# Kernel optimization log

Hardware: AMD Instinct MI355X
Metric: run time of the kernel (lower is better)

## Reference

```python
import jax, jax.numpy as jnp
import numpy as np

BS, SEQ, NV, DM, K = 128, 2048, 64, 512, 64
MAX_ITER, TOL = 10, 1e-4


def setup_inputs() -> dict:
    key = jax.random.key(0)
    k1, k2, k3, k4 = jax.random.split(key, 4)
    x = jax.random.normal(k1, (BS, SEQ, NV), jnp.float32)
    bound = 1.0 / np.sqrt(SEQ)
    W = jax.random.uniform(k2, (DM, SEQ), jnp.float32, -bound, bound)  # nn.Linear weight
    b = jax.random.uniform(k3, (DM,), jnp.float32, -bound, bound)
    centroids = jax.random.normal(k4, (K, DM), jnp.float32)  # kaiming-uniform-init param (random stand-in)
    return {"x": x, "W": W, "b": b, "centroids": centroids}


def _kmeans(x_emb, centroids):
    # x_emb: [N, DM]; fixed-length scan with a `done` flag emulating torch's tol break.
    N = x_emb.shape[0]
    x_sq = jnp.sum(x_emb * x_emb, axis=1, keepdims=True)  # [N,1]

    def body(state, _):
        cent, ids, done = state
        # squared euclidean distances (argmin-equivalent to cdist p=2)
        d2 = x_sq - 2.0 * (x_emb @ cent.T) + jnp.sum(cent * cent, axis=1)  # [N,K]
        new_ids = jnp.argmin(d2, axis=1)
        sums = jax.ops.segment_sum(x_emb, new_ids, num_segments=K)          # [K,DM]
        counts = jax.ops.segment_sum(jnp.ones((N,), x_emb.dtype), new_ids, num_segments=K)
        means = sums / jnp.maximum(counts, 1.0)[:, None]
        new_cent = jnp.where((counts > 0)[:, None], means, cent)  # empty cluster keeps old centroid
        shift = jnp.linalg.norm(new_cent - cent)
        cent_out = jnp.where(done, cent, new_cent)
        ids_out = jnp.where(done, ids, new_ids)
        done_out = done | (shift < TOL)
        return (cent_out, ids_out, done_out), None

    init = (centroids, jnp.zeros((N,), jnp.int32), jnp.array(False))
    (cent, ids, _), _ = jax.lax.scan(body, init, None, length=MAX_ITER)
    return ids, cent


def reference(x, W, b, centroids):
    # x: [bs, seq, n_vars] -> permute -> linear(seq->d_model) -> [bs*n_vars, d_model]
    xt = jnp.transpose(x, (0, 2, 1))                 # [bs, n_vars, seq]
    x_emb = (xt @ W.T + b).reshape(-1, DM)           # [bs*n_vars, d_model]
    ids, cent = _kmeans(x_emb, centroids)
    prob = jax.nn.one_hot(ids, K, dtype=jnp.float32).reshape(BS, NV, K)
    return prob, cent, x_emb
```

## Files before the change

### kernel.cpp

```cpp
#include <hip/hip_runtime.h>

#define SEQ 2048
#define NVAR 64
#define DMODEL 512
#define BSZ 128
#define KC 64
#define NPT (BSZ*NVAR)
#define MAXIT 10

typedef __bf16 bf16x8 __attribute__((ext_vector_type(8)));
typedef float f32x4 __attribute__((ext_vector_type(4)));

__device__ __forceinline__ void load_lds16(const void* g, void* l) {
  __builtin_amdgcn_global_load_lds((const __attribute__((address_space(1))) void*)g,
                                   (__attribute__((address_space(3))) void*)l, 16, 0, 0);
}

__device__ __forceinline__ unsigned short bf16_rn(float x) {
  unsigned int u = __float_as_uint(x);
  u += 0x7fffu + ((u >> 16) & 1u);
  return (unsigned short)(u >> 16);
}

__global__ __launch_bounds__(256) void init_k(const float* __restrict__ c0,
    float* __restrict__ cent, unsigned short* __restrict__ centh,
    unsigned short* __restrict__ centl, float* __restrict__ csq4,
    int* __restrict__ done, float* __restrict__ shift2, int* __restrict__ ticket) {
  const int k = blockIdx.x, t = threadIdx.x;
  __shared__ float red[256];
  float v0, v1;
  {
    int d = t;
    v0 = c0[k * DMODEL + d];
    cent[k * DMODEL + d] = v0;
    unsigned short h = bf16_rn(v0);
    centh[k * DMODEL + d] = h;
    centl[k * DMODEL + d] = bf16_rn(v0 - __uint_as_float((unsigned)h << 16));
  }
  {
    int d = t + 256;
    v1 = c0[k * DMODEL + d];
    cent[k * DMODEL + d] = v1;
    unsigned short h = bf16_rn(v1);
    centh[k * DMODEL + d] = h;
    centl[k * DMODEL + d] = bf16_rn(v1 - __uint_as_float((unsigned)h << 16));
  }
  red[t] = v0 * v0; __syncthreads();
  for (int s = 64; s > 0; s >>= 1) { if ((t & 127) < s) red[t] += red[t + s]; __syncthreads(); }
  if (t == 0)   csq4[0 * KC + k] = red[0];
  if (t == 128) csq4[1 * KC + k] = red[128];
  __syncthreads();
  red[t] = v1 * v1; __syncthreads();
  for (int s = 64; s > 0; s >>= 1) { if ((t & 127) < s) red[t] += red[t + s]; __syncthreads(); }
  if (t == 0)   csq4[2 * KC + k] = red[0];
  if (t == 128) csq4[3 * KC + k] = red[128];
  if (k == 0 && t < MAXIT) { shift2[t] = 0.f; ticket[t] = 0; }
  if (k == 0 && t == 31) *done = 0;
}

__global__ __launch_bounds__(256) void conv_w(const float* __restrict__ W,
    unsigned short* __restrict__ Wh, unsigned short* __restrict__ Wl) {
  int i = (blockIdx.x * 256 + threadIdx.x) * 4;
  float4 v = *(const float4*)(W + i);
  ushort4 h, l;
  h.x = bf16_rn(v.x); l.x = bf16_rn(v.x - __uint_as_float((unsigned)h.x << 16));
  h.y = bf16_rn(v.y); l.y = bf16_rn(v.y - __uint_as_float((unsigned)h.y << 16));
  h.z = bf16_rn(v.z); l.z = bf16_rn(v.z - __uint_as_float((unsigned)h.z << 16));
  h.w = bf16_rn(v.w); l.w = bf16_rn(v.w - __uint_as_float((unsigned)h.w << 16));
  *(ushort4*)(Wh + i) = h;
  *(ushort4*)(Wl + i) = l;
}

__global__ __launch_bounds__(256) void conv_x(const float* __restrict__ x,
    unsigned short* __restrict__ Xh, unsigned short* __restrict__ Xl) {
  __shared__ float tile[64 * 65];
  const int k0 = blockIdx.x * 64;
  const int bs = blockIdx.y;
  const int t = threadIdx.x;
  const float* xb = x + (size_t)bs * SEQ * NVAR + (size_t)k0 * NVAR;
  #pragma unroll
  for (int p = 0; p < 4; ++p) {
    int idx = t + 256 * p;
    int row = idx >> 4, c4 = (idx & 15) * 4;
    float4 v = *(const float4*)(xb + row * NVAR + c4);
    tile[row * 65 + c4 + 0] = v.x; tile[row * 65 + c4 + 1] = v.y;
    tile[row * 65 + c4 + 2] = v.z; tile[row * 65 + c4 + 3] = v.w;
  }
  __syncthreads();
  const int v = t >> 2;
  const int kc = (t & 3) * 16;
  unsigned short h[16], l[16];
  #pragma unroll
  for (int j = 0; j < 16; ++j) {
    float f = tile[(kc + j) * 65 + v];
    h[j] = bf16_rn(f);
    l[j] = bf16_rn(f - __uint_as_float((unsigned)h[j] << 16));
  }
  size_t off = (size_t)(bs * 64 + v) * SEQ + k0 + kc;
  *(uint4*)(Xh + off)     = *(uint4*)&h[0];
  *(uint4*)(Xh + off + 8) = *(uint4*)&h[8];
  *(uint4*)(Xl + off)     = *(uint4*)&l[0];
  *(uint4*)(Xl + off + 8) = *(uint4*)&l[8];
}

__global__ __launch_bounds__(256) void gemm_mfma(
    const unsigned short* __restrict__ Ah, const unsigned short* __restrict__ Al,
    const unsigned short* __restrict__ Bh, const unsigned short* __restrict__ Bl,
    const float* __restrict__ bias, float* __restrict__ emb) {
  __shared__ unsigned short sAh[32 * 64] __attribute__((aligned(16)));
  __shared__ unsigned short sAl[32 * 64] __attribute__((aligned(16)));
  __shared__ unsigned short sBh[256 * 64] __attribute__((aligned(16)));
  __shared__ unsigned short sBl[256 * 64] __attribute__((aligned(16)));
  const int t = threadIdx.x;
  const int w = t >> 6, lane = t & 63;
  const int m0 = blockIdx.x * 32;
  const int n0 = blockIdx.y * 256;
  const int wn = w * 64;
  const int lrow = lane >> 3, sl8 = lane & 7;
  const int csrc = sl8 ^ lrow;

  f32x4 acc[2][4];
  #pragma unroll
  for (int i = 0; i < 2; ++i)
    #pragma unroll
    for (int j = 0; j < 4; ++j) acc[i][j] = (f32x4){0.f, 0.f, 0.f, 0.f};

  for (int kt = 0; kt < SEQ; kt += 64) {
    __syncthreads();
    {
      const int r = w * 8 + lrow;
      const size_t ga = (size_t)(m0 + r) * SEQ + kt + csrc * 8;
      load_lds16(Ah + ga, &sAh[r * 64 + sl8 * 8]);
      load_lds16(Al + ga, &sAl[r * 64 + sl8 * 8]);
    }
    #pragma unroll
    for (int i = 0; i < 8; ++i) {
      const int r = w * 64 + i * 8 + lrow;
      const size_t gb = (size_t)(n0 + r) * SEQ + kt + csrc * 8;
      load_lds16(Bh + gb, &sBh[r * 64 + sl8 * 8]);
      load_lds16(Bl + gb, &sBl[r * 64 + sl8 * 8]);
    }
    __syncthreads();
    #pragma unroll
    for (int kk = 0; kk < 2; ++kk) {
      const int sl = ((kk * 4 + (lane >> 4)) ^ (lane & 7)) * 8;
      bf16x8 ah[2], al[2], bh[4], bl[4];
      #pragma unroll
      for (int mi = 0; mi < 2; ++mi) {
        int off = (mi * 16 + (lane & 15)) * 64 + sl;
        ah[mi] = *(const bf16x8*)&sAh[off];
        al[mi] = *(const bf16x8*)&sAl[off];
      }
      #pragma unroll
      for (int ni = 0; ni < 4; ++ni) {
        int off = (wn + ni * 16 + (lane & 15)) * 64 + sl;
        bh[ni] = *(const bf16x8*)&sBh[off];
        bl[ni] = *(const bf16x8*)&sBl[off];
      }
      #pragma unroll
      for (int mi = 0; mi < 2; ++mi)
        #pragma unroll
        for (int ni = 0; ni < 4; ++ni) {
          acc[mi][ni] = __builtin_amdgcn_mfma_f32_16x16x32_bf16(ah[mi], bh[ni], acc[mi][ni], 0, 0, 0);
          acc[mi][ni] = __builtin_amdgcn_mfma_f32_16x16x32_bf16(ah[mi], bl[ni], acc[mi][ni], 0, 0, 0);
          acc[mi][ni] = __builtin_amdgcn_mfma_f32_16x16x32_bf16(al[mi], bh[ni], acc[mi][ni], 0, 0, 0);
        }
    }
  }
  #pragma unroll
  for (int ni = 0; ni < 4; ++ni) {
    const int n = n0 + wn + ni * 16 + (lane & 15);
    const float bv = bias[n];
    #pragma unroll
    for (int mi = 0; mi < 2; ++mi) {
      const int m = m0 + mi * 16 + (lane >> 4) * 4;
      #pragma unroll
      for (int r = 0; r < 4; ++r)
        emb[(size_t)(m + r) * DMODEL + n] = acc[mi][ni][r] + bv;
    }
  }
}

__global__ __launch_bounds__(256) void gemm_emb(const float* __restrict__ x,
    const float* __restrict__ W, const float* __restrict__ bias,
    float* __restrict__ emb) {
  __shared__ float As[64][64];
  __shared__ float Ws[64][132];
  const int bs = blockIdx.y;
  const int n0 = blockIdx.x * 128;
  const int t = threadIdx.x;
  const int tx = t & 15, ty = t >> 4;
  float bv[8];
  #pragma unroll
  for (int j = 0; j < 8; ++j) bv[j] = bias[n0 + 8 * tx + j];
  float acc[4][8];
  #pragma unroll
  for (int i = 0; i < 4; ++i)
    #pragma unroll
    for (int j = 0; j < 8; ++j) acc[i][j] = 0.f;
  const float* xb = x + (size_t)bs * SEQ * NVAR;
  for (int k0 = 0; k0 < SEQ; k0 += 64) {
    __syncthreads();
    {
      const float4* src = (const float4*)(xb + (size_t)k0 * NVAR);
      float4* dst = (float4*)&As[0][0];
      #pragma unroll
      for (int r = 0; r < 4; ++r) dst[t + 256 * r] = src[t + 256 * r];
    }
    #pragma unroll
    for (int r = 0; r < 8; ++r) {
      int idx = t + 256 * r;
      int k4 = idx & 15, n = idx >> 4;
      float4 wv = *(const float4*)(W + (size_t)(n0 + n) * SEQ + k0 + 4 * k4);
      Ws[4 * k4 + 0][n] = wv.x; Ws[4 * k4 + 1][n] = wv.y;
      Ws[4 * k4 + 2][n] = wv.z; Ws[4 * k4 + 3][n] = wv.w;
    }
    __syncthreads();
    #pragma unroll 8
    for (int kk = 0; kk < 64; ++kk) {
      const float4 a  = *(const float4*)&As[kk][4 * ty];
      const float4 w0 = *(const float4*)&Ws[kk][8 * tx];
      const float4 w1 = *(const float4*)&Ws[kk][8 * tx + 4];
      const float av[4] = {a.x, a.y, a.z, a.w};
      const float wv[8] = {w0.x, w0.y, w0.z, w0.w, w1.x, w1.y, w1.z, w1.w};
      #pragma unroll
      for (int i = 0; i < 4; ++i)
        #pragma unroll
        for (int j = 0; j < 8; ++j)
          acc[i][j] = fmaf(av[i], wv[j], acc[i][j]);
    }
  }
  #pragma unroll
  for (int i = 0; i < 4; ++i) {
    int row = bs * NVAR + 4 * ty + i;
    float4 o0 = make_float4(acc[i][0] + bv[0], acc[i][1] + bv[1],
                            acc[i][2] + bv[2], acc[i][3] + bv[3]);
    float4 o1 = make_float4(acc[i][4] + bv[4], acc[i][5] + bv[5],
                            acc[i][6] + bv[6], acc[i][7] + bv[7]);
    *(float4*)(emb + (size_t)row * DMODEL + n0 + 8 * tx) = o0;
    *(float4*)(emb + (size_t)row * DMODEL + n0 + 8 * tx + 4) = o1;
  }
}

__global__ __launch_bounds__(256) void conv_et(const float* __restrict__ emb,
    unsigned short* __restrict__ Eh, unsigned short* __restrict__ El,
    unsigned short* __restrict__ Eth, unsigned short* __restrict__ Etl) {
  __shared__ unsigned short Lh[64][72];
  __shared__ unsigned short Ll[64][72];
  const int d0 = blockIdx.x * 64;
  const int p0 = blockIdx.y * 64;
  const int t = threadIdx.x;
  #pragma unroll
  for (int q = 0; q < 2; ++q) {
    int idx = t + 256 * q;
    int r = idx >> 3, c = idx & 7;
    const float* src = emb + (size_t)(p0 + r) * DMODEL + d0 + c * 8;
    float4 v0 = *(const float4*)src;
    float4 v1 = *(const float4*)(src + 4);
    unsigned short h[8], l[8];
    const float vv[8] = {v0.x, v0.y, v0.z, v0.w, v1.x, v1.y, v1.z, v1.w};
    #pragma unroll
    for (int j = 0; j < 8; ++j) {
      h[j] = bf16_rn(vv[j]);
      l[j] = bf16_rn(vv[j] - __uint_as_float((unsigned)h[j] << 16));
    }
    size_t eo = (size_t)(p0 + r) * DMODEL + d0 + c * 8;
    *(uint4*)(Eh + eo) = *(uint4*)&h[0];
    *(uint4*)(El + eo) = *(uint4*)&l[0];
    *(uint4*)&Lh[r][c * 8] = *(uint4*)&h[0];
    *(uint4*)&Ll[r][c * 8] = *(uint4*)&l[0];
  }
  __syncthreads();
  #pragma unroll
  for (int q = 0; q < 2; ++q) {
    int idx = t + 256 * q;
    int dd = idx >> 3, pc = idx & 7;
    unsigned short h[8], l[8];
    #pragma unroll
    for (int j = 0; j < 8; ++j) {
      h[j] = Lh[pc * 8 + j][dd];
      l[j] = Ll[pc * 8 + j][dd];
    }
    size_t to = (size_t)(d0 + dd) * NPT + p0 + pc * 8;
    *(uint4*)(Eth + to) = *(uint4*)&h[0];
    *(uint4*)(Etl + to) = *(uint4*)&l[0];
  }
}

__global__ __launch_bounds__(256) void k12_fused(
    const unsigned short* __restrict__ Eh, const unsigned short* __restrict__ El,
    const unsigned short* __restrict__ Eth, const unsigned short* __restrict__ Etl,
    const unsigned short* __restrict__ Ch, const unsigned short* __restrict__ Cl,
    const float* __restrict__ csq4, const int* __restrict__ done,
    int* __restrict__ ids, float* __restrict__ pcnt, float* __restrict__ psum) {
  if (*done) return;
  __shared__ __align__(16) unsigned char smem[98304];
  __shared__ float csq_l[64];
  __shared__ int cnt_l[64];
  __shared__ int ids_l[128];
  const int t = threadIdx.x;
  const int w = t >> 6, lane = t & 63;
  const int g = blockIdx.x & 63, dq = blockIdx.x >> 6;
  const int p0 = g * 128;
  const int lrow = lane >> 3, sl8 = lane & 7;
  const int csrc = sl8 ^ lrow;

  if (t < 64) {
    csq_l[t] = csq4[t] + csq4[KC + t] + csq4[2 * KC + t] + csq4[3 * KC + t];
    cnt_l[t] = 0;
  }
  __syncthreads();

#define STAGE_A(B, KT) do { \
    unsigned short* bEh = (unsigned short*)(smem + (B) * 49152); \
    unsigned short* bEl = (unsigned short*)(smem + (B) * 49152 + 16384); \
    unsigned short* bCh = (unsigned short*)(smem + (B) * 49152 + 32768); \
    unsigned short* bCl = (unsigned short*)(smem + (B) * 49152 + 40960); \
    _Pragma("unroll") \
    for (int i_ = 0; i_ < 4; ++i_) { \
      const int r_ = w * 32 + i_ * 8 + lrow; \
      const size_t ga_ = (size_t)(p0 + r_) * DMODEL + (KT) + csrc * 8; \
      load_lds16(Eh + ga_, &bEh[r_ * 64 + sl8 * 8]); \
      load_lds16(El + ga_, &bEl[r_ * 64 + sl8 * 8]); \
    } \
    _Pragma("unroll") \
    for (int i_ = 0; i_ < 2; ++i_) { \
      const int r_ = w * 16 + i_ * 8 + lrow; \
      const size_t gc_ = (size_t)r_ * DMODEL + (KT) + csrc * 8; \
      load_lds16(Ch + gc_, &bCh[r_ * 64 + sl8 * 8]); \
      load_lds16(Cl + gc_, &bCl[r_ * 64 + sl8 * 8]); \
    } \
  } while (0)

#define COMPUTE_A(B) do { \
    const unsigned short* bEh = (const unsigned short*)(smem + (B) * 49152); \
    const unsigned short* bEl = (const unsigned short*)(smem + (B) * 49152 + 16384); \
    const unsigned short* bCh = (const unsigned short*)(smem + (B) * 49152 + 32768); \
    const unsigned short* bCl = (const unsigned short*)(smem + (B) * 49152 + 40960); \
    _Pragma("unroll") \
    for (int kk = 0; kk < 2; ++kk) { \
      const int sl = ((kk * 4 + (lane >> 4)) ^ (lane & 7)) * 8; \
      bf16x8 eh[2], el[2], ch[4], cl[4]; \
      _Pragma("unroll") \
      for (int mi = 0; mi < 2; ++mi) { \
        int off = (w * 32 + mi * 16 + (lane & 15)) * 64 + sl; \
        eh[mi] = *(const bf16x8*)&bEh[off]; \
        el[mi] = *(const bf16x8*)&bEl[off]; \
      } \
      _Pragma("unroll") \
      for (int ni = 0; ni < 4; ++ni) { \
        int off = (ni * 16 + (lane & 15)) * 64 + sl; \
        ch[ni] = *(const bf16x8*)&bCh[off]; \
        cl[ni] = *(const bf16x8*)&bCl[off]; \
      } \
      _Pragma("unroll") \
      for (int mi = 0; mi < 2; ++mi) \
        _Pragma("unroll") \
        for (int ni = 0; ni < 4; ++ni) { \
          acc[mi][ni] = __builtin_amdgcn_mfma_f32_16x16x32_bf16(eh[mi], ch[ni], acc[mi][ni], 0, 0, 0); \
          acc[mi][ni] = __builtin_amdgcn_mfma_f32_16x16x32_bf16(eh[mi], cl[ni], acc[mi][ni], 0, 0, 0); \
          acc[mi][ni] = __builtin_amdgcn_mfma_f32_16x16x32_bf16(el[mi], ch[ni], acc[mi][ni], 0, 0, 0); \
        } \
    } \
  } while (0)

  f32x4 acc[2][4];
  #pragma unroll
  for (int i = 0; i < 2; ++i)
    #pragma unroll
    for (int j = 0; j < 4; ++j) acc[i][j] = (f32x4){0.f, 0.f, 0.f, 0.f};

  STAGE_A(0, 0);
  for (int kt8 = 0; kt8 < 8; kt8 += 2) {
    STAGE_A(1, (kt8 + 1) * 64);
    asm volatile("s_waitcnt vmcnt(12)" ::: "memory");
    __builtin_amdgcn_s_barrier();
    __builtin_amdgcn_sched_barrier(0);
    COMPUTE_A(0);
    __builtin_amdgcn_s_barrier();
    if (kt8 + 2 < 8) {
      STAGE_A(0, (kt8 + 2) * 64);
      asm volatile("s_waitcnt vmcnt(12)" ::: "memory");
    } else {
      asm volatile("s_waitcnt vmcnt(0)" ::: "memory");
    }
    __builtin_amdgcn_s_barrier();
    __builtin_amdgcn_sched_barrier(0);
    COMPUTE_A(1);
    __builtin_amdgcn_s_barrier();
  }

  #pragma unroll
  for (int mi = 0; mi < 2; ++mi) {
    #pragma unroll
    for (int r = 0; r < 4; ++r) {
      float bv = csq_l[lane & 15] - 2.f * acc[mi][0][r];
      int bk = lane & 15;
      #pragma unroll
      for (int ni = 1; ni < 4; ++ni) {
        const int k = ni * 16 + (lane & 15);
        float v = csq_l[k] - 2.f * acc[mi][ni][r];
        if (v < bv) { bv = v; bk = k; }
      }
      #pragma unroll
      for (int m = 1; m < 16; m <<= 1) {
        float ov = __shfl_xor(bv, m, 64);
        int   ok = __shfl_xor(bk, m, 64);
        if (ov < bv || (ov == bv && ok < bk)) { bv = ov; bk = ok; }
      }
      if ((lane & 15) == 0) {
        const int p = w * 32 + mi * 16 + (lane >> 4) * 4 + r;
        ids_l[p] = bk;
        atomicAdd(&cnt_l[bk], 1);
      }
    }
  }
  __syncthreads();
  if (dq == 0) {
    if (t < 128) ids[p0 + t] = ids_l[t];
    if (t < 64) pcnt[g * KC + t] = (float)cnt_l[t];
  }

#define STAGE_B(B, KT) do { \
    unsigned short* bTh = (unsigned short*)(smem + 17408 + (B) * 32768); \
    unsigned short* bTl = (unsigned short*)(smem + 17408 + (B) * 32768 + 16384); \
    _Pragma("unroll") \
    for (int i_ = 0; i_ < 4; ++i_) { \
      const int rr_ = w * 32 + i_ * 8 + lrow; \
      const size_t gt_ = (size_t)(dq * 128 + rr_) * NPT + g * 128 + (KT) + csrc * 8; \
      load_lds16(Eth + gt_, &bTh[rr_ * 64 + sl8 * 8]); \
      load_lds16(Etl + gt_, &bTl[rr_ * 64 + sl8 * 8]); \
    } \
  } while (0)

#define COMPUTE_B(B, KT) do { \
    const unsigned short* bTh = (const unsigned short*)(smem + 17408 + (B) * 32768); \
    const unsigned short* bTl = (const unsigned short*)(smem + 17408 + (B) * 32768 + 16384); \
    _Pragma("unroll") \
    for (int kk = 0; kk < 2; ++kk) { \
      const int quad = lane >> 4; \
      const int poff = (KT) + kk * 32 + quad * 8; \
      bf16x8 a[4], bh[2], bl[2]; \
      _Pragma("unroll") \
      for (int mi = 0; mi < 4; ++mi) \
        a[mi] = *(const bf16x8*)&sOH[(mi * 16 + (lane & 15)) * 136 + poff]; \
      const int sl = ((kk * 4 + quad) ^ (lane & 7)) * 8; \
      _Pragma("unroll") \
      for (int ni = 0; ni < 2; ++ni) { \
        int off = (w * 32 + ni * 16 + (lane & 15)) * 64 + sl; \
        bh[ni] = *(const bf16x8*)&bTh[off]; \
        bl[ni] = *(const bf16x8*)&bTl[off]; \
      } \
      _Pragma("unroll") \
      for (int mi = 0; mi < 4; ++mi) \
        _Pragma("unroll") \
        for (int ni = 0; ni < 2; ++ni) { \
          bcc[mi][ni] = __builtin_amdgcn_mfma_f32_16x16x32_bf16(a[mi], bh[ni], bcc[mi][ni], 0, 0, 0); \
          bcc[mi][ni] = __builtin_amdgcn_mfma_f32_16x16x32_bf16(a[mi], bl[ni], bcc[mi][ni], 0, 0, 0); \
        } \
    } \
  } while (0)

  {
    unsigned short* sOH = (unsigned short*)smem;
    STAGE_B(0, 0);
    #pragma unroll
    for (int q = 0; q < 4; ++q) {
      int c = t * 4 + q;
      int cl = c >> 4, pc = c & 15;
      unsigned short v[8];
      #pragma unroll
      for (int j = 0; j < 8; ++j)
        v[j] = (ids_l[pc * 8 + j] == cl) ? (unsigned short)0x3F80 : (unsigned short)0;
      *(uint4*)&sOH[cl * 136 + pc * 8] = *(uint4*)&v[0];
    }
    STAGE_B(1, 64);

    f32x4 bcc[4][2];
    #pragma unroll
    for (int i = 0; i < 4; ++i)
      #pragma unroll
      for (int j = 0; j < 2; ++j) bcc[i][j] = (f32x4){0.f, 0.f, 0.f, 0.f};

    asm volatile("s_waitcnt lgkmcnt(0)" ::: "memory");
    asm volatile("s_waitcnt vmcnt(8)" ::: "memory");
    __builtin_amdgcn_s_barrier();
    __builtin_amdgcn_sched_barrier(0);
    COMPUTE_B(0, 0);
    asm volatile("s_waitcnt vmcnt(0)" ::: "memory");
    __builtin_amdgcn_s_barrier();
    __builtin_amdgcn_sched_barrier(0);
    COMPUTE_B(1, 64);

    #pragma unroll
    for (int mi = 0; mi < 4; ++mi)
      #pragma unroll
      for (int ni = 0; ni < 2; ++ni) {
        const int cl = mi * 16 + (lane >> 4) * 4;
        const int d = dq * 128 + w * 32 + ni * 16 + (lane & 15);
        #pragma unroll
        for (int r = 0; r < 4; ++r)
          psum[((size_t)g * KC + cl + r) * DMODEL + d] = bcc[mi][ni][r];
      }
  }
#undef STAGE_A
#undef COMPUTE_A
#undef STAGE_B
#undef COMPUTE_B
}

__global__ __launch_bounds__(128) void k3_update(float* __restrict__ cent,
    unsigned short* __restrict__ centh, unsigned short* __restrict__ centl,
    const float* __restrict__ psum, const float* __restrict__ pcnt,
    int* __restrict__ done, float* __restrict__ csq4,
    float* __restrict__ shift2, int* __restrict__ ticket, int iter) {
  if (*done) return;
  const int bk = blockIdx.x & 63, dq = blockIdx.x >> 6;
  const int t = threadIdx.x;
  __shared__ float red[128];
  __shared__ float cnt_s;
  red[t] = (t < 64) ? pcnt[(size_t)t * KC + bk] : 0.f;
  __syncthreads();
  for (int s = 64; s > 0; s >>= 1) { if (t < s) red[t] += red[t + s]; __syncthreads(); }
  if (t == 0) cnt_s = red[0];
  __syncthreads();
  const float count = cnt_s;
  const int d = dq * 128 + t;
  float s = 0.f;
  #pragma unroll 16
  for (int g = 0; g < 64; ++g)
    s += psum[((size_t)g * KC + bk) * DMODEL + d];
  float oldv = cent[bk * DMODEL + d];
  float newv = (count > 0.f) ? (s / fmaxf(count, 1.f)) : oldv;
  cent[bk * DMODEL + d] = newv;
  unsigned short h = bf16_rn(newv);
  centh[bk * DMODEL + d] = h;
  centl[bk * DMODEL + d] = bf16_rn(newv - __uint_as_float((unsigned)h << 16));
  float df = newv - oldv;
  red[t] = df * df; __syncthreads();
  for (int s2 = 64; s2 > 0; s2 >>= 1) { if (t < s2) red[t] += red[t + s2]; __syncthreads(); }
  float tot_sh = red[0]; __syncthreads();
  red[t] = newv * newv; __syncthreads();
  for (int s2 = 64; s2 > 0; s2 >>= 1) { if (t < s2) red[t] += red[t + s2]; __syncthreads(); }
  if (t == 0) {
    csq4[dq * KC + bk] = red[0];
    atomicAdd(shift2 + iter, tot_sh);
    __threadfence();
    int tk = atomicAdd(ticket + iter, 1);
    if (tk == 255) {
      float tot = atomicAdd(shift2 + iter, 0.f);
      if (sqrtf(tot) < 1e-4f) *done = 1;
    }
  }
}

__global__ __launch_bounds__(256) void finalize_k(const int* __restrict__ ids,
    const float* __restrict__ cent, float* __restrict__ out) {
  int t = blockIdx.x * 256 + threadIdx.x;
  if (t < NPT * KC) {
    int n = t >> 6, k = t & 63;
    out[t] = (ids[n] == k) ? 1.f : 0.f;
  } else {
    int i = t - NPT * KC;
    if (i < KC * DMODEL) out[NPT * KC + i] = cent[i];
  }
}

extern "C" void kernel_launch(void* const* d_in, const int* in_sizes, int n_in,
                              void* d_out, int out_size, void* d_ws, size_t ws_size,
                              hipStream_t stream) {
  const float* x    = (const float*)d_in[0];
  const float* W    = (const float*)d_in[1];
  const float* bias = (const float*)d_in[2];
  const float* c0   = (const float*)d_in[3];
  float* out = (float*)d_out;
  float* emb_out = out + NPT * KC + KC * DMODEL;

  char* ws = (char*)d_ws;
  unsigned short* Ehi  = (unsigned short*)(ws + 0);
  unsigned short* Elo  = (unsigned short*)(ws + 8388608);
  unsigned short* Eth  = (unsigned short*)(ws + 16777216);
  unsigned short* Etl  = (unsigned short*)(ws + 25165824);
  float* psum    = (float*)(ws + 33554432);
  float* cent    = (float*)(ws + 41943040);
  unsigned short* centh = (unsigned short*)(ws + 42074112);
  unsigned short* centl = (unsigned short*)(ws + 42139648);
  float* csq4    = (float*)(ws + 42205184);
  float* shift2  = (float*)(ws + 42206208);
  int*   ticket  = (int*)(ws + 42206272);
  int*   done_f  = (int*)(ws + 42206336);
  float* pcnt    = (float*)(ws + 42206400);
  int*   ids     = (int*)(ws + 42271936);
  unsigned short* Xh = (unsigned short*)(ws + 0);
  unsigned short* Xl = (unsigned short*)(ws + 33554432);
  unsigned short* Wh = (unsigned short*)(ws + 67108864);
  unsigned short* Wl = (unsigned short*)(ws + 69206016);
  const size_t need_fast = 71303168;
  (void)n_in; (void)in_sizes; (void)out_size;

  if (ws_size >= need_fast) {
    conv_w<<<1024, 256, 0, stream>>>(W, Wh, Wl);
    conv_x<<<dim3(32, BSZ), 256, 0, stream>>>(x, Xh, Xl);
    gemm_mfma<<<dim3(256, 2), 256, 0, stream>>>(Xh, Xl, Wh, Wl, bias, emb_out);
  } else {
    gemm_emb<<<dim3(4, BSZ), 256, 0, stream>>>(x, W, bias, emb_out);
  }
  init_k<<<KC, 256, 0, stream>>>(c0, cent, centh, centl, csq4, done_f, shift2, ticket);
  conv_et<<<dim3(8, 128), 256, 0, stream>>>(emb_out, Ehi, Elo, Eth, Etl);
  for (int it = 0; it < MAXIT; ++it) {
    k12_fused<<<256, 256, 0, stream>>>(Ehi, Elo, Eth, Etl, centh, centl,
                                       csq4, done_f, ids, pcnt, psum);
    k3_update<<<256, 128, 0, stream>>>(cent, centh, centl, psum, pcnt, done_f,
                                       csq4, shift2, ticket, it);
  }
  finalize_k<<<2176, 256, 0, stream>>>(ids, cent, out);
}
```

Before: 494.8 us.

## Fuse k-means iterations into one cooperative persistent kernel with grid barriers

Replaces the 20 per-iteration kernel launches (assign+partial-sum and centroid update) plus finalize with a single cooperative kernel that loops over iterations and separates phases with a hand-rolled two-level atomic grid barrier. Blocks exit early when the shift drops below tolerance. This removes launch gaps and the early-return check kernels, at the cost of spin-wait barriers and a requirement that all 256 blocks with 96KB LDS each be co-resident. If the cooperative launch fails, it falls back to the old per-iteration path.

```diff
diff --git a/kernel.cpp b/kernel.cpp
--- a/kernel.cpp
+++ b/kernel.cpp
@@ -25,7 +25,8 @@
 __global__ __launch_bounds__(256) void init_k(const float* __restrict__ c0,
     float* __restrict__ cent, unsigned short* __restrict__ centh,
     unsigned short* __restrict__ centl, float* __restrict__ csq4,
-    int* __restrict__ done, float* __restrict__ shift2, int* __restrict__ ticket) {
+    int* __restrict__ done, float* __restrict__ shift2, int* __restrict__ ticket,
+    int* __restrict__ bar) {
   const int k = blockIdx.x, t = threadIdx.x;
   __shared__ float red[256];
   float v0, v1;
@@ -55,6 +56,7 @@
   if (t == 0)   csq4[2 * KC + k] = red[0];
   if (t == 128) csq4[3 * KC + k] = red[128];
   if (k == 0 && t < MAXIT) { shift2[t] = 0.f; ticket[t] = 0; }
+  if (k == 0) { bar[t] = 0; if (t < 64) bar[256 + t] = 0; }
   if (k == 0 && t == 31) *done = 0;
 }
 
@@ -285,6 +287,309 @@
     *(uint4*)(Eth + to) = *(uint4*)&h[0];
     *(uint4*)(Etl + to) = *(uint4*)&l[0];
   }
+}
+
+__global__ __launch_bounds__(256) void loop_k2(
+    const unsigned short* __restrict__ Eh, const unsigned short* __restrict__ El,
+    const unsigned short* __restrict__ Eth, const unsigned short* __restrict__ Etl,
+    unsigned short* __restrict__ Ch, unsigned short* __restrict__ Cl,
+    float* __restrict__ cent, float* __restrict__ csq4,
+    float* __restrict__ psum, float* __restrict__ pcnt,
+    int* __restrict__ ids, float* __restrict__ shift2,
+    float* __restrict__ out, int* __restrict__ bar) {
+  __shared__ __align__(16) unsigned char smem[98304];
+  __shared__ float csq_l[64];
+  __shared__ int cnt_l[64];
+  __shared__ int ids_l[128];
+  __shared__ float red[128];
+  __shared__ float cnt_s;
+  __shared__ float tot_s;
+  const int t = threadIdx.x;
+  const int bid = blockIdx.x;
+  const int w = t >> 6, lane = t & 63;
+  const int g = bid & 63, dq = bid >> 6;
+  const int p0 = g * 128;
+  const int lrow = lane >> 3, sl8 = lane & 7;
+  const int csrc = sl8 ^ lrow;
+  int nbar = 0;
+
+#define GRIDBAR() do { \
+    __threadfence(); \
+    __syncthreads(); \
+    if (t == 0) { \
+      int x_ = bid & 7; \
+      int p_ = __hip_atomic_fetch_add(&bar[x_ * 32], 1, __ATOMIC_RELAXED, __HIP_MEMORY_SCOPE_AGENT); \
+      if (p_ == nbar * 32 + 31) { \
+        int q_ = __hip_atomic_fetch_add(&bar[256], 1, __ATOMIC_RELAXED, __HIP_MEMORY_SCOPE_AGENT); \
+        if (q_ == nbar * 8 + 7) \
+          __hip_atomic_store(&bar[288], nbar + 1, __ATOMIC_RELAXED, __HIP_MEMORY_SCOPE_AGENT); \
+      } \
+      while (__hip_atomic_load(&bar[288], __ATOMIC_RELAXED, __HIP_MEMORY_SCOPE_AGENT) <= nbar) \
+        __builtin_amdgcn_s_sleep(2); \
+    } \
+    __syncthreads(); \
+    __threadfence(); \
+    nbar = nbar + 1; \
+  } while (0)
+
+#define LP_STAGE_A(B, KT) do { \
+    unsigned short* bEh = (unsigned short*)(smem + (B) * 49152); \
+    unsigned short* bEl = (unsigned short*)(smem + (B) * 49152 + 16384); \
+    unsigned short* bCh = (unsigned short*)(smem + (B) * 49152 + 32768); \
+    unsigned short* bCl = (unsigned short*)(smem + (B) * 49152 + 40960); \
+    _Pragma("unroll") \
+    for (int i_ = 0; i_ < 4; ++i_) { \
+      const int r_ = w * 32 + i_ * 8 + lrow; \
+      const size_t ga_ = (size_t)(p0 + r_) * DMODEL + (KT) + csrc * 8; \
+      load_lds16(Eh + ga_, &bEh[r_ * 64 + sl8 * 8]); \
+      load_lds16(El + ga_, &bEl[r_ * 64 + sl8 * 8]); \
+    } \
+    _Pragma("unroll") \
+    for (int i_ = 0; i_ < 2; ++i_) { \
+      const int r_ = w * 16 + i_ * 8 + lrow; \
+      const size_t gc_ = (size_t)r_ * DMODEL + (KT) + csrc * 8; \
+      load_lds16(Ch + gc_, &bCh[r_ * 64 + sl8 * 8]); \
+      load_lds16(Cl + gc_, &bCl[r_ * 64 + sl8 * 8]); \
+    } \
+  } while (0)
+
+#define LP_COMPUTE_A(B) do { \
+    const unsigned short* bEh = (const unsigned short*)(smem + (B) * 49152); \
+    const unsigned short* bEl = (const unsigned short*)(smem + (B) * 49152 + 16384); \
+    const unsigned short* bCh = (const unsigned short*)(smem + (B) * 49152 + 32768); \
+    const unsigned short* bCl = (const unsigned short*)(smem + (B) * 49152 + 40960); \
+    _Pragma("unroll") \
+    for (int kk = 0; kk < 2; ++kk) { \
+      const int sl = ((kk * 4 + (lane >> 4)) ^ (lane & 7)) * 8; \
+      bf16x8 eh[2], el[2], ch[4], cl[4]; \
+      _Pragma("unroll") \
+      for (int mi = 0; mi < 2; ++mi) { \
+        int off = (w * 32 + mi * 16 + (lane & 15)) * 64 + sl; \
+        eh[mi] = *(const bf16x8*)&bEh[off]; \
+        el[mi] = *(const bf16x8*)&bEl[off]; \
+      } \
+      _Pragma("unroll") \
+      for (int ni = 0; ni < 4; ++ni) { \
+        int off = (ni * 16 + (lane & 15)) * 64 + sl; \
+        ch[ni] = *(const bf16x8*)&bCh[off]; \
+        cl[ni] = *(const bf16x8*)&bCl[off]; \
+      } \
+      _Pragma("unroll") \
+      for (int mi = 0; mi < 2; ++mi) \
+        _Pragma("unroll") \
+        for (int ni = 0; ni < 4; ++ni) { \
+          acc[mi][ni] = __builtin_amdgcn_mfma_f32_16x16x32_bf16(eh[mi], ch[ni], acc[mi][ni], 0, 0, 0); \
+          acc[mi][ni] = __builtin_amdgcn_mfma_f32_16x16x32_bf16(eh[mi], cl[ni], acc[mi][ni], 0, 0, 0); \
+          acc[mi][ni] = __builtin_amdgcn_mfma_f32_16x16x32_bf16(el[mi], ch[ni], acc[mi][ni], 0, 0, 0); \
+        } \
+    } \
+  } while (0)
+
+#define LP_STAGE_B(B, KT) do { \
+    unsigned short* bTh = (unsigned short*)(smem + 17408 + (B) * 32768); \
+    unsigned short* bTl = (unsigned short*)(smem + 17408 + (B) * 32768 + 16384); \
+    _Pragma("unroll") \
+    for (int i_ = 0; i_ < 4; ++i_) { \
+      const int rr_ = w * 32 + i_ * 8 + lrow; \
+      const size_t gt_ = (size_t)(dq * 128 + rr_) * NPT + g * 128 + (KT) + csrc * 8; \
+      load_lds16(Eth + gt_, &bTh[rr_ * 64 + sl8 * 8]); \
+      load_lds16(Etl + gt_, &bTl[rr_ * 64 + sl8 * 8]); \
+    } \
+  } while (0)
+
+#define LP_COMPUTE_B(B, KT) do { \
+    const unsigned short* bTh = (const unsigned short*)(smem + 17408 + (B) * 32768); \
+    const unsigned short* bTl = (const unsigned short*)(smem + 17408 + (B) * 32768 + 16384); \
+    _Pragma("unroll") \
+    for (int kk = 0; kk < 2; ++kk) { \
+      const int quad = lane >> 4; \
+      const int poff = (KT) + kk * 32 + quad * 8; \
+      bf16x8 a[4], bh[2], bl[2]; \
+      _Pragma("unroll") \
+      for (int mi = 0; mi < 4; ++mi) \
+        a[mi] = *(const bf16x8*)&sOH[(mi * 16 + (lane & 15)) * 136 + poff]; \
+      const int sl = ((kk * 4 + quad) ^ (lane & 7)) * 8; \
+      _Pragma("unroll") \
+      for (int ni = 0; ni < 2; ++ni) { \
+        int off = (w * 32 + ni * 16 + (lane & 15)) * 64 + sl; \
+        bh[ni] = *(const bf16x8*)&bTh[off]; \
+        bl[ni] = *(const bf16x8*)&bTl[off]; \
+      } \
+      _Pragma("unroll") \
+      for (int mi = 0; mi < 4; ++mi) \
+        _Pragma("unroll") \
+        for (int ni = 0; ni < 2; ++ni) { \
+          bcc[mi][ni] = __builtin_amdgcn_mfma_f32_16x16x32_bf16(a[mi], bh[ni], bcc[mi][ni], 0, 0, 0); \
+          bcc[mi][ni] = __builtin_amdgcn_mfma_f32_16x16x32_bf16(a[mi], bl[ni], bcc[mi][ni], 0, 0, 0); \
+        } \
+    } \
+  } while (0)
+
+  for (int it = 0; it < MAXIT; ++it) {
+    if (t < 64) {
+      csq_l[t] = csq4[t] + csq4[KC + t] + csq4[2 * KC + t] + csq4[3 * KC + t];
+      cnt_l[t] = 0;
+    }
+    __syncthreads();
+
+    f32x4 acc[2][4];
+    #pragma unroll
+    for (int i = 0; i < 2; ++i)
+      #pragma unroll
+      for (int j = 0; j < 4; ++j) acc[i][j] = (f32x4){0.f, 0.f, 0.f, 0.f};
+
+    LP_STAGE_A(0, 0);
+    for (int kt8 = 0; kt8 < 8; kt8 += 2) {
+      LP_STAGE_A(1, (kt8 + 1) * 64);
+      asm volatile("s_waitcnt vmcnt(12)" ::: "memory");
+      __builtin_amdgcn_s_barrier();
+      __builtin_amdgcn_sched_barrier(0);
+      LP_COMPUTE_A(0);
+      __builtin_amdgcn_s_barrier();
+      if (kt8 + 2 < 8) {
+        LP_STAGE_A(0, (kt8 + 2) * 64);
+        asm volatile("s_waitcnt vmcnt(12)" ::: "memory");
+      } else {
+        asm volatile("s_waitcnt vmcnt(0)" ::: "memory");
+      }
+      __builtin_amdgcn_s_barrier();
+      __builtin_amdgcn_sched_barrier(0);
+      LP_COMPUTE_A(1);
+      __builtin_amdgcn_s_barrier();
+    }
+
+    #pragma unroll
+    for (int mi = 0; mi < 2; ++mi) {
+      #pragma unroll
+      for (int r = 0; r < 4; ++r) {
+        float bv = csq_l[lane & 15] - 2.f * acc[mi][0][r];
+        int bk = lane & 15;
+        #pragma unroll
+        for (int ni = 1; ni < 4; ++ni) {
+          const int k = ni * 16 + (lane & 15);
+          float v = csq_l[k] - 2.f * acc[mi][ni][r];
+          if (v < bv) { bv = v; bk = k; }
+        }
+        #pragma unroll
+        for (int m = 1; m < 16; m <<= 1) {
+          float ov = __shfl_xor(bv, m, 64);
+          int   ok = __shfl_xor(bk, m, 64);
+          if (ov < bv || (ov == bv && ok < bk)) { bv = ov; bk = ok; }
+        }
+        if ((lane & 15) == 0) {
+          const int p = w * 32 + mi * 16 + (lane >> 4) * 4 + r;
+          ids_l[p] = bk;
+          atomicAdd(&cnt_l[bk], 1);
+        }
+      }
+    }
+    __syncthreads();
+    if (dq == 0 && t < 64) pcnt[g * KC + t] = (float)cnt_l[t];
+
+    {
+      unsigned short* sOH = (unsigned short*)smem;
+      LP_STAGE_B(0, 0);
+      #pragma unroll
+      for (int q = 0; q < 4; ++q) {
+        int c = t * 4 + q;
+        int cl = c >> 4, pc = c & 15;
+        unsigned short v[8];
+        #pragma unroll
+        for (int j = 0; j < 8; ++j)
+          v[j] = (ids_l[pc * 8 + j] == cl) ? (unsigned short)0x3F80 : (unsigned short)0;
+        *(uint4*)&sOH[cl * 136 + pc * 8] = *(uint4*)&v[0];
+      }
+      LP_STAGE_B(1, 64);
+
+      f32x4 bcc[4][2];
+      #pragma unroll
+      for (int i = 0; i < 4; ++i)
+        #pragma unroll
+        for (int j = 0; j < 2; ++j) bcc[i][j] = (f32x4){0.f, 0.f, 0.f, 0.f};
+
+      asm volatile("s_waitcnt lgkmcnt(0)" ::: "memory");
+      asm volatile("s_waitcnt vmcnt(8)" ::: "memory");
+      __builtin_amdgcn_s_barrier();
+      __builtin_amdgcn_sched_barrier(0);
+      LP_COMPUTE_B(0, 0);
+      asm volatile("s_waitcnt vmcnt(0)" ::: "memory");
+      __builtin_amdgcn_s_barrier();
+      __builtin_amdgcn_sched_barrier(0);
+      LP_COMPUTE_B(1, 64);
+
+      #pragma unroll
+      for (int mi = 0; mi < 4; ++mi)
+        #pragma unroll
+        for (int ni = 0; ni < 2; ++ni) {
+          const int cl = mi * 16 + (lane >> 4) * 4;
+          const int d = dq * 128 + w * 32 + ni * 16 + (lane & 15);
+          #pragma unroll
+          for (int r = 0; r < 4; ++r)
+            psum[((size_t)g * KC + cl + r) * DMODEL + d] = bcc[mi][ni][r];
+        }
+    }
+    GRIDBAR();
+
+    {
+      const int bk = bid & 63, dqq = bid >> 6;
+      if (t < 128) red[t] = (t < 64) ? pcnt[(size_t)t * KC + bk] : 0.f;
+      __syncthreads();
+      for (int s = 64; s > 0; s >>= 1) { if (t < s) red[t] += red[t + s]; __syncthreads(); }
+      if (t == 0) cnt_s = red[0];
+      __syncthreads();
+      const float count = cnt_s;
+      float df2 = 0.f, sq = 0.f;
+      if (t < 128) {
+        const int d = dqq * 128 + t;
+        float s = 0.f;
+        #pragma unroll 16
+        for (int g2 = 0; g2 < 64; ++g2)
+          s += psum[((size_t)g2 * KC + bk) * DMODEL + d];
+        float oldv = cent[bk * DMODEL + d];
+        float newv = (count > 0.f) ? (s / fmaxf(count, 1.f)) : oldv;
+        cent[bk * DMODEL + d] = newv;
+        unsigned short h = bf16_rn(newv);
+        Ch[bk * DMODEL + d] = h;
+        Cl[bk * DMODEL + d] = bf16_rn(newv - __uint_as_float((unsigned)h << 16));
+        float df = newv - oldv;
+        df2 = df * df; sq = newv * newv;
+      }
+      if (t < 128) red[t] = df2;
+      __syncthreads();
+      for (int s2 = 64; s2 > 0; s2 >>= 1) { if (t < s2) red[t] += red[t + s2]; __syncthreads(); }
+      if (t == 0) atomicAdd(shift2 + it, red[0]);
+      __syncthreads();
+      if (t < 128) red[t] = sq;
+      __syncthreads();
+      for (int s2 = 64; s2 > 0; s2 >>= 1) { if (t < s2) red[t] += red[t + s2]; __syncthreads(); }
+      if (t == 0) csq4[dqq * KC + bk] = red[0];
+    }
+    GRIDBAR();
+
+    if (t == 0) tot_s = shift2[it];
+    __syncthreads();
+    if (sqrtf(tot_s) < 1e-4f) break;
+  }
+
+  if (dq == 0 && t < 128) ids[p0 + t] = ids_l[t];
+  GRIDBAR();
+  {
+    const int gtid = bid * 256 + t;
+    const int n = gtid >> 3;
+    const int k0 = (gtid & 7) * 8;
+    const int idn = ids[n];
+    float v[8];
+    #pragma unroll
+    for (int j = 0; j < 8; ++j) v[j] = (idn == k0 + j) ? 1.f : 0.f;
+    *(float4*)(out + (size_t)n * KC + k0)     = make_float4(v[0], v[1], v[2], v[3]);
+    *(float4*)(out + (size_t)n * KC + k0 + 4) = make_float4(v[4], v[5], v[6], v[7]);
+    if (gtid < KC * DMODEL) out[NPT * KC + gtid] = cent[gtid];
+  }
+#undef GRIDBAR
+#undef LP_STAGE_A
+#undef LP_COMPUTE_A
+#undef LP_STAGE_B
+#undef LP_COMPUTE_B
 }
 
 __global__ __launch_bounds__(256) void k12_fused(
@@ -591,6 +896,7 @@
   int*   done_f  = (int*)(ws + 42206336);
   float* pcnt    = (float*)(ws + 42206400);
   int*   ids     = (int*)(ws + 42271936);
+  int*   bar     = (int*)(ws + 42304704);
   unsigned short* Xh = (unsigned short*)(ws + 0);
   unsigned short* Xl = (unsigned short*)(ws + 33554432);
   unsigned short* Wh = (unsigned short*)(ws + 67108864);
@@ -605,13 +911,23 @@
   } else {
     gemm_emb<<<dim3(4, BSZ), 256, 0, stream>>>(x, W, bias, emb_out);
   }
-  init_k<<<KC, 256, 0, stream>>>(c0, cent, centh, centl, csq4, done_f, shift2, ticket);
+  init_k<<<KC, 256, 0, stream>>>(c0, cent, centh, centl, csq4, done_f, shift2,
+                                 ticket, bar);
   conv_et<<<dim3(8, 128), 256, 0, stream>>>(emb_out, Ehi, Elo, Eth, Etl);
-  for (int it = 0; it < MAXIT; ++it) {
-    k12_fused<<<256, 256, 0, stream>>>(Ehi, Elo, Eth, Etl, centh, centl,
-                                       csq4, done_f, ids, pcnt, psum);
-    k3_update<<<256, 128, 0, stream>>>(cent, centh, centl, psum, pcnt, done_f,
-                                       csq4, shift2, ticket, it);
-  }
-  finalize_k<<<2176, 256, 0, stream>>>(ids, cent, out);
-}
+
+  void* cargs[] = {(void*)&Ehi, (void*)&Elo, (void*)&Eth, (void*)&Etl,
+                   (void*)&centh, (void*)&centl, (void*)&cent, (void*)&csq4,
+                   (void*)&psum, (void*)&pcnt, (void*)&ids, (void*)&shift2,
+                   (void*)&out, (void*)&bar};
+  hipError_t cerr = hipLaunchCooperativeKernel(loop_k2, dim3(256), dim3(256),
+                                               cargs, 0u, stream);
+  if (cerr != hipSuccess) {
+    for (int it = 0; it < MAXIT; ++it) {
+      k12_fused<<<256, 256, 0, stream>>>(Ehi, Elo, Eth, Etl, centh, centl,
+                                         csq4, done_f, ids, pcnt, psum);
+      k3_update<<<256, 128, 0, stream>>>(cent, centh, centl, psum, pcnt, done_f,
+                                         csq4, shift2, ticket, it);
+    }
+    finalize_k<<<2176, 256, 0, stream>>>(ids, cent, out);
+  }
+}
```

After: 1.279 ms. 158% more time.
